# Performance work log

Measured on AMD Instinct MI355X. Metric: run time of the kernel, lower is better.

Reference implementation:

```python
import jax, jax.numpy as jnp
import numpy as np

N_HEAD = 16

def setup_inputs() -> dict:
    key = jax.random.key(0)
    ks = jax.random.split(key, 5)
    C = 1024
    x = jax.random.normal(ks[0], (2, 2048, C), dtype=jnp.float32)
    w_attn = jax.random.normal(ks[1], (C, 3 * C), dtype=jnp.float32) * (C ** -0.5)
    b_attn = jax.random.normal(ks[2], (3 * C,), dtype=jnp.float32) * 0.02
    w_proj = jax.random.normal(ks[3], (C, C), dtype=jnp.float32) * (C ** -0.5)
    b_proj = jax.random.normal(ks[4], (C,), dtype=jnp.float32) * 0.02
    return {"x": x, "w_attn": w_attn, "b_attn": b_attn, "w_proj": w_proj, "b_proj": b_proj}

def reference(x, w_attn, b_attn, w_proj, b_proj):
    B, T, C = x.shape
    H = N_HEAD
    D = C // H  # head_dim
    qkv = x @ w_attn + b_attn  # [B,T,3C]
    q, k, v = jnp.split(qkv, 3, axis=-1)
    # [B,T,H,D] -> [B,H,T,D]
    q = q.reshape(B, T, H, D).transpose(0, 2, 1, 3)
    k = k.reshape(B, T, H, D).transpose(0, 2, 1, 3)
    v = v.reshape(B, T, H, D).transpose(0, 2, 1, 3)
    scale = 1.0 / np.sqrt(D).astype(np.float32)
    att = jnp.einsum('bhqd,bhkd->bhqk', q, k) * scale  # [B,H,T,T]
    causal = jnp.tril(jnp.ones((T, T), dtype=bool))
    att = jnp.where(causal, att, jnp.finfo(att.dtype).min)
    att = jax.nn.softmax(att, axis=-1)
    y = jnp.einsum('bhqk,bhkd->bhqd', att, v)  # [B,H,T,D]
    y = y.transpose(0, 2, 1, 3).reshape(B, T, C)
    return y @ w_proj + b_proj
```

## Files before the change

### kernel.cpp

```cpp
#include <hip/hip_runtime.h>
#include <hip/hip_bf16.h>
#include <stdint.h>

typedef __bf16 bf16x8 __attribute__((ext_vector_type(8)));
typedef __bf16 bf16x4 __attribute__((ext_vector_type(4)));
typedef float  f32x4  __attribute__((ext_vector_type(4)));
typedef float  f32x16 __attribute__((ext_vector_type(16)));

#define GLOBAL_AS __attribute__((address_space(1)))
#define LDS_AS    __attribute__((address_space(3)))

__device__ __forceinline__ void gld_lds16(const __bf16* g, __bf16* l) {
  __builtin_amdgcn_global_load_lds((GLOBAL_AS void*)g, (LDS_AS void*)l, 16, 0, 0);
}

#define QSCALE 0.18033688011116029f

__device__ __forceinline__ unsigned pk2(float a, float b) {
  unsigned short ua = __builtin_bit_cast(unsigned short, (__bf16)a);
  unsigned short ub = __builtin_bit_cast(unsigned short, (__bf16)b);
  return (unsigned)ua | ((unsigned)ub << 16);
}

union PackU { unsigned u[4]; bf16x8 v; };

__global__ __launch_bounds__(256)
void prep_kernel(const float* __restrict__ x, __bf16* __restrict__ xb,
                 const float* __restrict__ wa, __bf16* __restrict__ waT,
                 const float* __restrict__ wp, __bf16* __restrict__ wpT)
{
  const int id = blockIdx.x;
  const int tid = threadIdx.x;
  if (id < 2048) {
    int i = (id * 256 + tid) * 8;
    float4 a = *(const float4*)(x + i);
    float4 b = *(const float4*)(x + i + 4);
    bf16x8 o;
    o[0]=(__bf16)a.x; o[1]=(__bf16)a.y; o[2]=(__bf16)a.z; o[3]=(__bf16)a.w;
    o[4]=(__bf16)b.x; o[5]=(__bf16)b.y; o[6]=(__bf16)b.z; o[7]=(__bf16)b.w;
    *(bf16x8*)(xb + i) = o;
    return;
  }
  __shared__ float tile[32][33];
  const float* src; __bf16* dst; int R, C, c0, r0;
  if (id < 5120) {
    int idx = id - 2048;
    src = wa; dst = waT; R = 1024; C = 3072;
    c0 = (idx % 96) * 32; r0 = (idx / 96) * 32;
  } else {
    int idx = id - 5120;
    src = wp; dst = wpT; R = 1024; C = 1024;
    c0 = (idx & 31) * 32; r0 = (idx >> 5) * 32;
  }
  int tx = tid & 31, ty = tid >> 5;
  #pragma unroll
  for (int i = 0; i < 32; i += 8)
    tile[ty + i][tx] = src[(size_t)(r0 + ty + i) * C + (c0 + tx)];
  __syncthreads();
  #pragma unroll
  for (int i = 0; i < 32; i += 8)
    dst[(size_t)(c0 + ty + i) * R + (r0 + tx)] = (__bf16)tile[tx][ty + i];
}

template<int MODE, int BM>
__global__ __launch_bounds__(256, (BM == 128 ? 3 : 2))
void gemm_kernel(const __bf16* __restrict__ A,
                 const __bf16* __restrict__ Bt,
                 const float*  __restrict__ bias,
                 float* __restrict__ outF,
                 __bf16* __restrict__ qb,
                 __bf16* __restrict__ kb,
                 __bf16* __restrict__ vb,
                 int M, int N, int K)
{
  __shared__ __bf16 As[BM * 64];
  __shared__ __bf16 Bs[128 * 64];
  const int tid  = threadIdx.x;
  const int wave = tid >> 6, lane = tid & 63;
  const int l31 = lane & 31, hi = lane >> 5;
  int bm, bn;
  if (MODE == 0) {
    int bid = blockIdx.x;
    int bm_i = (bid & 7) * 4 + ((bid >> 3) & 3);
    int bn_i = bid >> 5;
    bm = bm_i * 128; bn = bn_i * 128;
  } else {
    bm = blockIdx.y * BM; bn = blockIdx.x * 128;
  }
  const int wr = (wave >> 1) * (BM / 2);
  const int wc = (wave & 1) * 64;
  constexpr int MT = BM / 64;

  f32x16 acc[MT][2] = {};

  const int nkt = K >> 6;
  for (int kt = 0; kt < nkt; ++kt) {
    const int k0 = kt << 6;
    __syncthreads();
    #pragma unroll
    for (int j = 0; j < BM / 32; ++j) {
      int c = j * 256 + tid;
      int r = c >> 3, cc = c & 7;
      int cs = cc ^ (r & 7);
      gld_lds16(A + (size_t)(bm + r) * K + (k0 + cs * 8), As + c * 8);
    }
    #pragma unroll
    for (int j = 0; j < 4; ++j) {
      int c = j * 256 + tid;
      int r = c >> 3, cc = c & 7;
      int cs = cc ^ (r & 7);
      gld_lds16(Bt + (size_t)(bn + r) * K + (k0 + cs * 8), Bs + c * 8);
    }
    __syncthreads();
    #pragma unroll
    for (int kk = 0; kk < 4; ++kk) {
      bf16x8 af[MT], bfr[2];
      #pragma unroll
      for (int mt = 0; mt < MT; ++mt) {
        int row = wr + mt * 32 + l31;
        int ch = (kk * 2 + hi) ^ (row & 7);
        af[mt] = *(const bf16x8*)(As + row * 64 + ch * 8);
      }
      #pragma unroll
      for (int nt = 0; nt < 2; ++nt) {
        int row = wc + nt * 32 + l31;
        int ch = (kk * 2 + hi) ^ (row & 7);
        bfr[nt] = *(const bf16x8*)(Bs + row * 64 + ch * 8);
      }
      #pragma unroll
      for (int mt = 0; mt < MT; ++mt)
        #pragma unroll
        for (int nt = 0; nt < 2; ++nt)
          acc[mt][nt] = __builtin_amdgcn_mfma_f32_32x32x16_bf16(af[mt], bfr[nt], acc[mt][nt], 0, 0, 0);
    }
  }

  float bv[2];
  #pragma unroll
  for (int nt = 0; nt < 2; ++nt) bv[nt] = bias[bn + wc + nt * 32 + l31];

  if (MODE == 1) {
    #pragma unroll
    for (int mt = 0; mt < MT; ++mt)
      #pragma unroll
      for (int nt = 0; nt < 2; ++nt) {
        int col = bn + wc + nt * 32 + l31;
        #pragma unroll
        for (int q2 = 0; q2 < 4; ++q2) {
          int rbase = bm + wr + mt * 32 + 8 * q2 + 4 * hi;
          #pragma unroll
          for (int j = 0; j < 4; ++j)
            outF[(size_t)(rbase + j) * N + col] = acc[mt][nt][q2 * 4 + j] + bv[nt];
        }
      }
  } else {
    #pragma unroll
    for (int mt = 0; mt < MT; ++mt) {
      #pragma unroll
      for (int q2 = 0; q2 < 4; ++q2) {
        const int tbase = bm + wr + mt * 32 + 8 * q2 + 4 * hi;
        const int b = tbase >> 11, t = tbase & 2047;
        #pragma unroll
        for (int nt = 0; nt < 2; ++nt) {
          int n = bn + wc + nt * 32 + l31;
          int sel = n >> 10, hd = n & 1023;
          int h = hd >> 6, d = hd & 63;
          size_t bh = (size_t)(b * 16 + h);
          if (sel == 2) {
            bf16x4 pv;
            #pragma unroll
            for (int j = 0; j < 4; ++j) pv[j] = (__bf16)(acc[mt][nt][q2 * 4 + j] + bv[nt]);
            *(bf16x4*)(vb + (bh * 64 + d) * 2048 + t) = pv;
          } else if (sel == 0) {
            #pragma unroll
            for (int j = 0; j < 4; ++j)
              qb[(bh * 2048 + (size_t)(t + j)) * 64 + d] =
                  (__bf16)((acc[mt][nt][q2 * 4 + j] + bv[nt]) * QSCALE);
          } else {
            #pragma unroll
            for (int j = 0; j < 4; ++j)
              kb[(bh * 2048 + (size_t)(t + j)) * 64 + d] =
                  (__bf16)(acc[mt][nt][q2 * 4 + j] + bv[nt]);
          }
        }
      }
    }
  }
}

__global__ __launch_bounds__(256, 4)
void attn_kernel(const __bf16* __restrict__ qg_, const __bf16* __restrict__ kg,
                 const __bf16* __restrict__ vg, __bf16* __restrict__ yg,
                 __bf16* __restrict__ pY, float* __restrict__ pL)
{
  const int n = blockIdx.x;
  const int xcd = n & 7;
  const int m = n >> 3;
  const int bh = xcd + 8 * (m & 3);
  const int t = m >> 2;
  const int b = bh >> 4, h = bh & 15;

  const int tid  = threadIdx.x;
  const int wave = tid >> 6;
  const int lane = tid & 63;
  const int l15  = lane & 15;
  const int g    = lane >> 4;
  const int sw   = l15 & 7;

  __shared__ __bf16 Kb[2][64 * 64];
  __shared__ __bf16 Vb[2][64 * 64];

  const __bf16* qbase = qg_ + (size_t)bh * 2048 * 64;
  const __bf16* kbase = kg  + (size_t)bh * 2048 * 64;
  const __bf16* vbase = vg  + (size_t)bh * 64 * 2048;

  bf16x8 qf0, qf1;
  f32x4 o0, o1, o2, o3, osum;

  bf16x8 ones;
  #pragma unroll
  for (int j = 0; j < 8; ++j) ones[j] = (__bf16)1.0f;

  auto LOADQ = [&](int strip) {
    const int q16 = strip * 64 + wave * 16 + l15;
    qf0 = *(const bf16x8*)(qbase + (size_t)q16 * 64 + g * 8);
    qf1 = *(const bf16x8*)(qbase + (size_t)q16 * 64 + 32 + g * 8);
  };
  auto RESET = [&]() {
    o0 = f32x4{}; o1 = f32x4{}; o2 = f32x4{}; o3 = f32x4{}; osum = f32x4{};
  };
  auto STAGE = [&](int kt, int bsel) {
    #pragma unroll
    for (int j = 0; j < 2; ++j) {
      int c = j * 256 + tid;
      int cr = c >> 3, cc = c & 7;
      int cs = cc ^ (cr & 7);
      int pr = (cr & 0x23) | ((cr & 0x10) >> 2) | ((cr & 0x0C) << 1);
      gld_lds16(kbase + (size_t)(kt * 64 + pr) * 64 + cs * 8, &Kb[bsel][0] + c * 8);
      gld_lds16(vbase + (size_t)cr * 2048 + (kt * 64 + cs * 8), &Vb[bsel][0] + c * 8);
    }
  };

  auto TILE = [&](int cur, bool diag) {
    const __bf16* KL = &Kb[cur][0];
    f32x4 s0 = {}, s1 = {}, s2 = {}, s3 = {};
    {
      bf16x8 k00 = *(const bf16x8*)(KL + (0  + l15) * 64 + ((0 + g) ^ sw) * 8);
      bf16x8 k01 = *(const bf16x8*)(KL + (0  + l15) * 64 + ((4 + g) ^ sw) * 8);
      bf16x8 k10 = *(const bf16x8*)(KL + (16 + l15) * 64 + ((0 + g) ^ sw) * 8);
      bf16x8 k11 = *(const bf16x8*)(KL + (16 + l15) * 64 + ((4 + g) ^ sw) * 8);
      bf16x8 k20 = *(const bf16x8*)(KL + (32 + l15) * 64 + ((0 + g) ^ sw) * 8);
      bf16x8 k21 = *(const bf16x8*)(KL + (32 + l15) * 64 + ((4 + g) ^ sw) * 8);
      bf16x8 k30 = *(const bf16x8*)(KL + (48 + l15) * 64 + ((0 + g) ^ sw) * 8);
      bf16x8 k31 = *(const bf16x8*)(KL + (48 + l15) * 64 + ((4 + g) ^ sw) * 8);
      __builtin_amdgcn_s_setprio(1);
      s0 = __builtin_amdgcn_mfma_f32_16x16x32_bf16(k00, qf0, s0, 0, 0, 0);
      s0 = __builtin_amdgcn_mfma_f32_16x16x32_bf16(k01, qf1, s0, 0, 0, 0);
      s1 = __builtin_amdgcn_mfma_f32_16x16x32_bf16(k10, qf0, s1, 0, 0, 0);
      s1 = __builtin_amdgcn_mfma_f32_16x16x32_bf16(k11, qf1, s1, 0, 0, 0);
      s2 = __builtin_amdgcn_mfma_f32_16x16x32_bf16(k20, qf0, s2, 0, 0, 0);
      s2 = __builtin_amdgcn_mfma_f32_16x16x32_bf16(k21, qf1, s2, 0, 0, 0);
      s3 = __builtin_amdgcn_mfma_f32_16x16x32_bf16(k30, qf0, s3, 0, 0, 0);
      s3 = __builtin_amdgcn_mfma_f32_16x16x32_bf16(k31, qf1, s3, 0, 0, 0);
      __builtin_amdgcn_s_setprio(0);
    }

    if (diag) {
      const int qr = wave * 16 + l15;
      #pragma unroll
      for (int r2 = 0; r2 < 4; ++r2) {
        if (8 * g + r2          > qr) s0[r2] = -3.0e38f;
        if (8 * g + 4 + r2      > qr) s1[r2] = -3.0e38f;
        if (32 + 8 * g + r2     > qr) s2[r2] = -3.0e38f;
        if (32 + 8 * g + 4 + r2 > qr) s3[r2] = -3.0e38f;
      }
    }

    #pragma unroll
    for (int r2 = 0; r2 < 4; ++r2) s0[r2] = exp2f(s0[r2]);
    #pragma unroll
    for (int r2 = 0; r2 < 4; ++r2) s1[r2] = exp2f(s1[r2]);
    #pragma unroll
    for (int r2 = 0; r2 < 4; ++r2) s2[r2] = exp2f(s2[r2]);
    #pragma unroll
    for (int r2 = 0; r2 < 4; ++r2) s3[r2] = exp2f(s3[r2]);

    PackU pa0, pa1;
    pa0.u[0] = pk2(s0[0], s0[1]); pa0.u[1] = pk2(s0[2], s0[3]);
    pa0.u[2] = pk2(s1[0], s1[1]); pa0.u[3] = pk2(s1[2], s1[3]);
    pa1.u[0] = pk2(s2[0], s2[1]); pa1.u[1] = pk2(s2[2], s2[3]);
    pa1.u[2] = pk2(s3[0], s3[1]); pa1.u[3] = pk2(s3[2], s3[3]);

    const __bf16* VL = &Vb[cur][0];
    bf16x8 v00 = *(const bf16x8*)(VL + (0  + l15) * 64 + ((0 + g) ^ sw) * 8);
    bf16x8 v01 = *(const bf16x8*)(VL + (0  + l15) * 64 + ((4 + g) ^ sw) * 8);
    bf16x8 v10 = *(const bf16x8*)(VL + (16 + l15) * 64 + ((0 + g) ^ sw) * 8);
    bf16x8 v11 = *(const bf16x8*)(VL + (16 + l15) * 64 + ((4 + g) ^ sw) * 8);
    bf16x8 v20 = *(const bf16x8*)(VL + (32 + l15) * 64 + ((0 + g) ^ sw) * 8);
    bf16x8 v21 = *(const bf16x8*)(VL + (32 + l15) * 64 + ((4 + g) ^ sw) * 8);
    bf16x8 v30 = *(const bf16x8*)(VL + (48 + l15) * 64 + ((0 + g) ^ sw) * 8);
    bf16x8 v31 = *(const bf16x8*)(VL + (48 + l15) * 64 + ((4 + g) ^ sw) * 8);

    __builtin_amdgcn_s_setprio(1);
    osum = __builtin_amdgcn_mfma_f32_16x16x32_bf16(pa0.v, ones, osum, 0, 0, 0);
    osum = __builtin_amdgcn_mfma_f32_16x16x32_bf16(pa1.v, ones, osum, 0, 0, 0);
    o0 = __builtin_amdgcn_mfma_f32_16x16x32_bf16(pa0.v, v00, o0, 0, 0, 0);
    o0 = __builtin_amdgcn_mfma_f32_16x16x32_bf16(pa1.v, v01, o0, 0, 0, 0);
    o1 = __builtin_amdgcn_mfma_f32_16x16x32_bf16(pa0.v, v10, o1, 0, 0, 0);
    o1 = __builtin_amdgcn_mfma_f32_16x16x32_bf16(pa1.v, v11, o1, 0, 0, 0);
    o2 = __builtin_amdgcn_mfma_f32_16x16x32_bf16(pa0.v, v20, o2, 0, 0, 0);
    o2 = __builtin_amdgcn_mfma_f32_16x16x32_bf16(pa1.v, v21, o2, 0, 0, 0);
    o3 = __builtin_amdgcn_mfma_f32_16x16x32_bf16(pa0.v, v30, o3, 0, 0, 0);
    o3 = __builtin_amdgcn_mfma_f32_16x16x32_bf16(pa1.v, v31, o3, 0, 0, 0);
    __builtin_amdgcn_s_setprio(0);
  };

  auto WRITE_Y = [&](int strip) {
    #pragma unroll
    for (int r2 = 0; r2 < 4; ++r2) {
      float il = 1.0f / osum[r2];
      int trow = strip * 64 + wave * 16 + 4 * g + r2;
      __bf16* dst = yg + ((size_t)(b * 2048 + trow)) * 1024 + h * 64;
      dst[l15]      = (__bf16)(o0[r2] * il);
      dst[16 + l15] = (__bf16)(o1[r2] * il);
      dst[32 + l15] = (__bf16)(o2[r2] * il);
      dst[48 + l15] = (__bf16)(o3[r2] * il);
    }
  };
  auto WRITE_PART = [&](int slot) {
    __bf16* po = pY + (size_t)slot * 4096;
    #pragma unroll
    for (int r2 = 0; r2 < 4; ++r2) {
      int row = wave * 16 + 4 * g + r2;
      __bf16* dst = po + row * 64;
      dst[l15]      = (__bf16)o0[r2];
      dst[16 + l15] = (__bf16)o1[r2];
      dst[32 + l15] = (__bf16)o2[r2];
      dst[48 + l15] = (__bf16)o3[r2];
    }
    if (l15 == 0) {
      #pragma unroll
      for (int r2 = 0; r2 < 4; ++r2)
        pL[slot * 64 + wave * 16 + 4 * g + r2] = osum[r2];
    }
  };

  int cur = 0;
  if (t < 16) {
    LOADQ(t); RESET();
    bf16x8 qB0, qB1;
    {
      const int q16b = (31 - t) * 64 + wave * 16 + l15;
      qB0 = *(const bf16x8*)(qbase + (size_t)q16b * 64 + g * 8);
      qB1 = *(const bf16x8*)(qbase + (size_t)q16b * 64 + 32 + g * 8);
    }
    STAGE(0, 0);
    for (int j = 0; j < 17; ++j) {
      __syncthreads();
      if (j < 16) {
        int nx = j + 1;
        STAGE((nx <= t) ? nx : (nx + 15 - t), cur ^ 1);
      }
      if (j <= t) {
        TILE(cur, j == t);
        if (j == t) { WRITE_Y(t); qf0 = qB0; qf1 = qB1; RESET(); }
      } else {
        TILE(cur, j == 16);
      }
      cur ^= 1;
    }
    WRITE_PART((bh * 16 + (15 - t)) * 2 + 1);
  } else {
    LOADQ(t); RESET();
    STAGE(0, 0);
    for (int j = 0; j < 16; ++j) {
      __syncthreads();
      if (j < 15) STAGE(j + 1, cur ^ 1);
      TILE(cur, false);
      cur ^= 1;
    }
    WRITE_PART((bh * 16 + (t - 16)) * 2);
  }
}

__global__ __launch_bounds__(256)
void attn_merge_kernel(const __bf16* __restrict__ pY, const float* __restrict__ pL,
                       __bf16* __restrict__ yg)
{
  const int us = blockIdx.x & 15, bh = blockIdx.x >> 4;
  const int b = bh >> 4, h = bh & 15;
  const int tid = threadIdx.x;
  const int row = tid >> 2, d0 = (tid & 3) * 16;
  const int slotA = (bh * 16 + us) * 2, slotB = slotA + 1;

  float l = pL[slotA * 64 + row] + pL[slotB * 64 + row];
  float inv = 1.0f / l;

  const __bf16* pa = pY + (size_t)slotA * 4096 + row * 64 + d0;
  const __bf16* pb = pY + (size_t)slotB * 4096 + row * 64 + d0;
  __bf16* dst = yg + ((size_t)(b * 2048 + (16 + us) * 64 + row)) * 1024 + h * 64 + d0;

  bf16x8 a0 = *(const bf16x8*)pa, a1 = *(const bf16x8*)(pa + 8);
  bf16x8 b0 = *(const bf16x8*)pb, b1 = *(const bf16x8*)(pb + 8);
  bf16x8 r0, r1;
  #pragma unroll
  for (int j = 0; j < 8; ++j) {
    r0[j] = (__bf16)(((float)a0[j] + (float)b0[j]) * inv);
    r1[j] = (__bf16)(((float)a1[j] + (float)b1[j]) * inv);
  }
  *(bf16x8*)dst = r0;
  *(bf16x8*)(dst + 8) = r1;
}

extern "C" void kernel_launch(void* const* d_in, const int* in_sizes, int n_in,
                              void* d_out, int out_size, void* d_ws, size_t ws_size,
                              hipStream_t stream)
{
  const float* x      = (const float*)d_in[0];
  const float* w_attn = (const float*)d_in[1];
  const float* b_attn = (const float*)d_in[2];
  const float* w_proj = (const float*)d_in[3];
  const float* b_proj = (const float*)d_in[4];
  float* out = (float*)d_out;

  __bf16* xb  = (__bf16*)d_ws;
  __bf16* waT = xb  + (size_t)4096 * 1024;
  __bf16* wpT = waT + (size_t)3072 * 1024;
  __bf16* qb  = wpT + (size_t)1024 * 1024;
  __bf16* kb  = qb  + (size_t)32 * 2048 * 64;
  __bf16* vb  = kb  + (size_t)32 * 2048 * 64;
  __bf16* yb  = vb  + (size_t)32 * 2048 * 64;

  __bf16* pY = xb;
  float*  pL = (float*)waT;

  prep_kernel<<<6144, 256, 0, stream>>>(x, xb, w_attn, waT, w_proj, wpT);
  gemm_kernel<0, 128><<<768, 256, 0, stream>>>(xb, waT, b_attn, nullptr,
                                               qb, kb, vb, 4096, 3072, 1024);
  attn_kernel<<<1024, 256, 0, stream>>>(qb, kb, vb, yb, pY, pL);
  attn_merge_kernel<<<512, 256, 0, stream>>>(pY, pL, yb);
  gemm_kernel<1, 64><<<dim3(8, 64), 256, 0, stream>>>(yb, wpT, b_proj, out,
                                                      nullptr, nullptr, nullptr, 4096, 1024, 1024);
}
```

Measured before the change: 100.0 us.

## Halve attention KV tile to 32 keys and raise occupancy to 8 blocks

Shrinks the K/V shared-memory tiles from 64 to 32 keys, which halves LDS per block and lets launch bounds request 8 blocks per CU instead of 4. The loop schedule is rewritten to walk twice as many smaller tiles. The diagonal mask now splits into two half-tiles, and the upper half is skipped entirely for waves whose rows lie fully below it. V staging uses a new swizzle for the 32-wide layout. In exchange there are twice as many barriers and MFMA chains half as long per sync, and the tighter register cap may cause spills.

Result: slower. 119.0 us (+19.0%).

```diff
diff --git a/kernel.cpp b/kernel.cpp
--- a/kernel.cpp
+++ b/kernel.cpp
@@ -188,7 +188,7 @@
   }
 }
 
-__global__ __launch_bounds__(256, 4)
+__global__ __launch_bounds__(256, 8)
 void attn_kernel(const __bf16* __restrict__ qg_, const __bf16* __restrict__ kg,
                  const __bf16* __restrict__ vg, __bf16* __restrict__ yg,
                  __bf16* __restrict__ pY, float* __restrict__ pL)
@@ -207,8 +207,8 @@
   const int g    = lane >> 4;
   const int sw   = l15 & 7;
 
-  __shared__ __bf16 Kb[2][64 * 64];
-  __shared__ __bf16 Vb[2][64 * 64];
+  __shared__ __bf16 Kb[2][32 * 64];
+  __shared__ __bf16 Vb[2][64 * 32];
 
   const __bf16* qbase = qg_ + (size_t)bh * 2048 * 64;
   const __bf16* kbase = kg  + (size_t)bh * 2048 * 64;
@@ -230,88 +230,60 @@
     o0 = f32x4{}; o1 = f32x4{}; o2 = f32x4{}; o3 = f32x4{}; osum = f32x4{};
   };
   auto STAGE = [&](int kt, int bsel) {
-    #pragma unroll
-    for (int j = 0; j < 2; ++j) {
-      int c = j * 256 + tid;
-      int cr = c >> 3, cc = c & 7;
-      int cs = cc ^ (cr & 7);
-      int pr = (cr & 0x23) | ((cr & 0x10) >> 2) | ((cr & 0x0C) << 1);
-      gld_lds16(kbase + (size_t)(kt * 64 + pr) * 64 + cs * 8, &Kb[bsel][0] + c * 8);
-      gld_lds16(vbase + (size_t)cr * 2048 + (kt * 64 + cs * 8), &Vb[bsel][0] + c * 8);
-    }
-  };
-
-  auto TILE = [&](int cur, bool diag) {
+    int c = tid;
+    int cr = c >> 3, cc = c & 7;
+    int cs = cc ^ (cr & 7);
+    int pr = (cr & 3) | ((cr & 0x10) >> 2) | ((cr & 0x0C) << 1);
+    gld_lds16(kbase + (size_t)(kt * 32 + pr) * 64 + cs * 8, &Kb[bsel][0] + c * 8);
+    int d = c >> 2, sl = c & 3;
+    int cs2 = sl ^ (d & 3);
+    gld_lds16(vbase + (size_t)d * 2048 + kt * 32 + cs2 * 8, &Vb[bsel][0] + c * 8);
+  };
+
+  auto TILE = [&](int cur, int dg) {
     const __bf16* KL = &Kb[cur][0];
-    f32x4 s0 = {}, s1 = {}, s2 = {}, s3 = {};
-    {
-      bf16x8 k00 = *(const bf16x8*)(KL + (0  + l15) * 64 + ((0 + g) ^ sw) * 8);
-      bf16x8 k01 = *(const bf16x8*)(KL + (0  + l15) * 64 + ((4 + g) ^ sw) * 8);
-      bf16x8 k10 = *(const bf16x8*)(KL + (16 + l15) * 64 + ((0 + g) ^ sw) * 8);
-      bf16x8 k11 = *(const bf16x8*)(KL + (16 + l15) * 64 + ((4 + g) ^ sw) * 8);
-      bf16x8 k20 = *(const bf16x8*)(KL + (32 + l15) * 64 + ((0 + g) ^ sw) * 8);
-      bf16x8 k21 = *(const bf16x8*)(KL + (32 + l15) * 64 + ((4 + g) ^ sw) * 8);
-      bf16x8 k30 = *(const bf16x8*)(KL + (48 + l15) * 64 + ((0 + g) ^ sw) * 8);
-      bf16x8 k31 = *(const bf16x8*)(KL + (48 + l15) * 64 + ((4 + g) ^ sw) * 8);
-      __builtin_amdgcn_s_setprio(1);
-      s0 = __builtin_amdgcn_mfma_f32_16x16x32_bf16(k00, qf0, s0, 0, 0, 0);
-      s0 = __builtin_amdgcn_mfma_f32_16x16x32_bf16(k01, qf1, s0, 0, 0, 0);
-      s1 = __builtin_amdgcn_mfma_f32_16x16x32_bf16(k10, qf0, s1, 0, 0, 0);
-      s1 = __builtin_amdgcn_mfma_f32_16x16x32_bf16(k11, qf1, s1, 0, 0, 0);
-      s2 = __builtin_amdgcn_mfma_f32_16x16x32_bf16(k20, qf0, s2, 0, 0, 0);
-      s2 = __builtin_amdgcn_mfma_f32_16x16x32_bf16(k21, qf1, s2, 0, 0, 0);
-      s3 = __builtin_amdgcn_mfma_f32_16x16x32_bf16(k30, qf0, s3, 0, 0, 0);
-      s3 = __builtin_amdgcn_mfma_f32_16x16x32_bf16(k31, qf1, s3, 0, 0, 0);
-      __builtin_amdgcn_s_setprio(0);
-    }
-
-    if (diag) {
+    f32x4 s0 = {}, s1 = {};
+    bf16x8 k00 = *(const bf16x8*)(KL + (0  + l15) * 64 + ((0 + g) ^ sw) * 8);
+    bf16x8 k01 = *(const bf16x8*)(KL + (0  + l15) * 64 + ((4 + g) ^ sw) * 8);
+    bf16x8 k10 = *(const bf16x8*)(KL + (16 + l15) * 64 + ((0 + g) ^ sw) * 8);
+    bf16x8 k11 = *(const bf16x8*)(KL + (16 + l15) * 64 + ((4 + g) ^ sw) * 8);
+    __builtin_amdgcn_s_setprio(1);
+    s0 = __builtin_amdgcn_mfma_f32_16x16x32_bf16(k00, qf0, s0, 0, 0, 0);
+    s0 = __builtin_amdgcn_mfma_f32_16x16x32_bf16(k01, qf1, s0, 0, 0, 0);
+    s1 = __builtin_amdgcn_mfma_f32_16x16x32_bf16(k10, qf0, s1, 0, 0, 0);
+    s1 = __builtin_amdgcn_mfma_f32_16x16x32_bf16(k11, qf1, s1, 0, 0, 0);
+    __builtin_amdgcn_s_setprio(0);
+
+    if (dg) {
+      const int off = (dg == 2) ? 32 : 0;
       const int qr = wave * 16 + l15;
       #pragma unroll
       for (int r2 = 0; r2 < 4; ++r2) {
-        if (8 * g + r2          > qr) s0[r2] = -3.0e38f;
-        if (8 * g + 4 + r2      > qr) s1[r2] = -3.0e38f;
-        if (32 + 8 * g + r2     > qr) s2[r2] = -3.0e38f;
-        if (32 + 8 * g + 4 + r2 > qr) s3[r2] = -3.0e38f;
+        if (off + 8 * g + r2     > qr) s0[r2] = -3.0e38f;
+        if (off + 8 * g + 4 + r2 > qr) s1[r2] = -3.0e38f;
       }
     }
 
     #pragma unroll
-    for (int r2 = 0; r2 < 4; ++r2) s0[r2] = exp2f(s0[r2]);
-    #pragma unroll
-    for (int r2 = 0; r2 < 4; ++r2) s1[r2] = exp2f(s1[r2]);
-    #pragma unroll
-    for (int r2 = 0; r2 < 4; ++r2) s2[r2] = exp2f(s2[r2]);
-    #pragma unroll
-    for (int r2 = 0; r2 < 4; ++r2) s3[r2] = exp2f(s3[r2]);
-
-    PackU pa0, pa1;
-    pa0.u[0] = pk2(s0[0], s0[1]); pa0.u[1] = pk2(s0[2], s0[3]);
-    pa0.u[2] = pk2(s1[0], s1[1]); pa0.u[3] = pk2(s1[2], s1[3]);
-    pa1.u[0] = pk2(s2[0], s2[1]); pa1.u[1] = pk2(s2[2], s2[3]);
-    pa1.u[2] = pk2(s3[0], s3[1]); pa1.u[3] = pk2(s3[2], s3[3]);
+    for (int r2 = 0; r2 < 4; ++r2) { s0[r2] = exp2f(s0[r2]); s1[r2] = exp2f(s1[r2]); }
+
+    PackU pa;
+    pa.u[0] = pk2(s0[0], s0[1]); pa.u[1] = pk2(s0[2], s0[3]);
+    pa.u[2] = pk2(s1[0], s1[1]); pa.u[3] = pk2(s1[2], s1[3]);
 
     const __bf16* VL = &Vb[cur][0];
-    bf16x8 v00 = *(const bf16x8*)(VL + (0  + l15) * 64 + ((0 + g) ^ sw) * 8);
-    bf16x8 v01 = *(const bf16x8*)(VL + (0  + l15) * 64 + ((4 + g) ^ sw) * 8);
-    bf16x8 v10 = *(const bf16x8*)(VL + (16 + l15) * 64 + ((0 + g) ^ sw) * 8);
-    bf16x8 v11 = *(const bf16x8*)(VL + (16 + l15) * 64 + ((4 + g) ^ sw) * 8);
-    bf16x8 v20 = *(const bf16x8*)(VL + (32 + l15) * 64 + ((0 + g) ^ sw) * 8);
-    bf16x8 v21 = *(const bf16x8*)(VL + (32 + l15) * 64 + ((4 + g) ^ sw) * 8);
-    bf16x8 v30 = *(const bf16x8*)(VL + (48 + l15) * 64 + ((0 + g) ^ sw) * 8);
-    bf16x8 v31 = *(const bf16x8*)(VL + (48 + l15) * 64 + ((4 + g) ^ sw) * 8);
+    const int vc = (g ^ (l15 & 3)) * 8;
+    bf16x8 v0 = *(const bf16x8*)(VL + (0  + l15) * 32 + vc);
+    bf16x8 v1 = *(const bf16x8*)(VL + (16 + l15) * 32 + vc);
+    bf16x8 v2 = *(const bf16x8*)(VL + (32 + l15) * 32 + vc);
+    bf16x8 v3 = *(const bf16x8*)(VL + (48 + l15) * 32 + vc);
 
     __builtin_amdgcn_s_setprio(1);
-    osum = __builtin_amdgcn_mfma_f32_16x16x32_bf16(pa0.v, ones, osum, 0, 0, 0);
-    osum = __builtin_amdgcn_mfma_f32_16x16x32_bf16(pa1.v, ones, osum, 0, 0, 0);
-    o0 = __builtin_amdgcn_mfma_f32_16x16x32_bf16(pa0.v, v00, o0, 0, 0, 0);
-    o0 = __builtin_amdgcn_mfma_f32_16x16x32_bf16(pa1.v, v01, o0, 0, 0, 0);
-    o1 = __builtin_amdgcn_mfma_f32_16x16x32_bf16(pa0.v, v10, o1, 0, 0, 0);
-    o1 = __builtin_amdgcn_mfma_f32_16x16x32_bf16(pa1.v, v11, o1, 0, 0, 0);
-    o2 = __builtin_amdgcn_mfma_f32_16x16x32_bf16(pa0.v, v20, o2, 0, 0, 0);
-    o2 = __builtin_amdgcn_mfma_f32_16x16x32_bf16(pa1.v, v21, o2, 0, 0, 0);
-    o3 = __builtin_amdgcn_mfma_f32_16x16x32_bf16(pa0.v, v30, o3, 0, 0, 0);
-    o3 = __builtin_amdgcn_mfma_f32_16x16x32_bf16(pa1.v, v31, o3, 0, 0, 0);
+    osum = __builtin_amdgcn_mfma_f32_16x16x32_bf16(pa.v, ones, osum, 0, 0, 0);
+    o0 = __builtin_amdgcn_mfma_f32_16x16x32_bf16(pa.v, v0, o0, 0, 0, 0);
+    o1 = __builtin_amdgcn_mfma_f32_16x16x32_bf16(pa.v, v1, o1, 0, 0, 0);
+    o2 = __builtin_amdgcn_mfma_f32_16x16x32_bf16(pa.v, v2, o2, 0, 0, 0);
+    o3 = __builtin_amdgcn_mfma_f32_16x16x32_bf16(pa.v, v3, o3, 0, 0, 0);
     __builtin_amdgcn_s_setprio(0);
   };
 
@@ -347,36 +319,30 @@
 
   int cur = 0;
   if (t < 16) {
+    const int sB = 31 - t;
+    const int nA = 2 * t + 2;
+    auto kvn = [&](int j) { return (j < nA) ? j : (32 + j - nA); };
     LOADQ(t); RESET();
-    bf16x8 qB0, qB1;
-    {
-      const int q16b = (31 - t) * 64 + wave * 16 + l15;
-      qB0 = *(const bf16x8*)(qbase + (size_t)q16b * 64 + g * 8);
-      qB1 = *(const bf16x8*)(qbase + (size_t)q16b * 64 + 32 + g * 8);
-    }
-    STAGE(0, 0);
-    for (int j = 0; j < 17; ++j) {
+    STAGE(kvn(0), 0);
+    for (int j = 0; j < 34; ++j) {
       __syncthreads();
-      if (j < 16) {
-        int nx = j + 1;
-        STAGE((nx <= t) ? nx : (nx + 15 - t), cur ^ 1);
-      }
-      if (j <= t) {
-        TILE(cur, j == t);
-        if (j == t) { WRITE_Y(t); qf0 = qB0; qf1 = qB1; RESET(); }
-      } else {
-        TILE(cur, j == 16);
-      }
+      if (j < 33) STAGE(kvn(j + 1), cur ^ 1);
+      const int jj = kvn(j);
+      int dg = 0;
+      if (j < nA) { if (jj == 2 * t) dg = 1; else if (jj == 2 * t + 1) dg = 2; }
+      else        { if (jj == 2 * sB) dg = 1; else if (jj == 2 * sB + 1) dg = 2; }
+      if (!(dg == 2 && wave < 2)) TILE(cur, dg);
+      if (j == nA - 1) { WRITE_Y(t); LOADQ(sB); RESET(); }
       cur ^= 1;
     }
     WRITE_PART((bh * 16 + (15 - t)) * 2 + 1);
   } else {
     LOADQ(t); RESET();
     STAGE(0, 0);
-    for (int j = 0; j < 16; ++j) {
+    for (int j = 0; j < 32; ++j) {
       __syncthreads();
-      if (j < 15) STAGE(j + 1, cur ^ 1);
-      TILE(cur, false);
+      if (j < 31) STAGE(j + 1, cur ^ 1);
+      TILE(cur, 0);
       cur ^= 1;
     }
     WRITE_PART((bh * 16 + (t - 16)) * 2);
```
